# Kernel optimization log

Measured on AMD Instinct MI355X. Metric: run time of the kernel, lower is better.

The kernel has to match this reference:

```python
import jax, jax.numpy as jnp
import numpy as np

SR = 44100
D = SR * 30          # duration_samples = 1_323_000
N = 1024             # number of note events
L = 32768            # max note length in samples
W = 1024             # hann window length (module's window_length)
H = 8                # harmonics in the synth
K = 128              # FIR taps in the effect chain
LAT = 2              # time_latent_size


def setup_inputs() -> dict:
    key = jax.random.key(0)
    ks = jax.random.split(key, 10)
    freq_rad = jax.random.uniform(ks[0], (N,), jnp.float32, 0.01, 0.3)
    velocity = jax.random.uniform(ks[1], (N,), jnp.float32, 1.0, 127.0)
    starts = jax.random.randint(ks[2], (N,), 0, D - L, dtype=jnp.int32)
    lengths = jax.random.randint(ks[3], (N,), 2048, L + 1, dtype=jnp.int32)
    # time_embedder: Linear(1,32) -> ReLU -> Linear(32,LAT)
    w1 = jax.random.normal(ks[4], (1, 32), jnp.float32)
    b1 = jnp.zeros((32,), jnp.float32)
    w2 = jax.random.normal(ks[5], (32, LAT), jnp.float32) / jnp.sqrt(32.0)
    b2 = jnp.zeros((LAT,), jnp.float32)
    # synth amplitude MLP: [freq, vel, latent] (2+LAT) -> 64 -> H
    ws1 = jax.random.normal(ks[6], (2 + LAT, 64), jnp.float32)
    bs1 = jnp.zeros((64,), jnp.float32)
    ws2 = jax.random.normal(ks[7], (64, H), jnp.float32) / 8.0
    bs2 = jnp.zeros((H,), jnp.float32)
    # effect chain: causal FIR (OIW layout) + tanh
    fir = jax.random.normal(ks[8], (1, 1, K), jnp.float32) / K
    return dict(freq_rad=freq_rad, velocity=velocity,
                w1=w1, b1=b1, w2=w2, b2=b2,
                ws1=ws1, bs1=bs1, ws2=ws2, bs2=bs2, fir=fir,
                starts=starts, lengths=lengths, duration_samples=D)


def reference(freq_rad, velocity, w1, b1, w2, b2, ws1, bs1, ws2, bs2, fir,
              starts, lengths, duration_samples):
    Dn = int(duration_samples)
    t = jnp.arange(L, dtype=jnp.float32)            # [L]
    ti = jnp.arange(L, dtype=jnp.int32)             # [L]
    ends = starts + lengths
    # output_length = min(end, duration) - start, clipped to [0, L]
    out_len = jnp.clip(jnp.minimum(ends, Dn) - starts, 0, L)  # [N]
    # time latent: MLP on normalized start time
    nt = (starts.astype(jnp.float32) / Dn)[:, None]           # [N,1]
    lat = jax.nn.relu(nt @ w1 + b1) @ w2 + b2                  # [N,LAT]
    vel = (velocity / 127.0)[:, None]                          # [N,1]
    # harmonic amplitudes from tiny MLP (the 'synth')
    feat = jnp.concatenate([freq_rad[:, None], vel, lat], axis=-1)  # [N,2+LAT]
    amps = jax.nn.softplus(jax.nn.relu(feat @ ws1 + bs1) @ ws2 + bs2)  # [N,H]
    # additive synthesis; fixed small loop over harmonics, vectorized over [N,L]
    phase = freq_rad[:, None] * t[None, :]                     # [N,L]
    seg = jnp.zeros((N, L), jnp.float32)
    for hh in range(1, H + 1):
        seg = seg + amps[:, hh - 1:hh] * jnp.sin(hh * phase)
    seg = seg * vel
    # hann window (torch periodic) on the LAST W samples of each variable-length segment
    n = jnp.arange(W, dtype=jnp.float32)
    hann = 0.5 * (1.0 - jnp.cos(2.0 * jnp.pi * n / W))         # [W]
    wpos = ti[None, :] - (out_len[:, None] - W)                # [N,L]
    in_win = (wpos >= 0) & (wpos < W)
    factor = jnp.where(in_win, hann[jnp.clip(wpos, 0, W - 1)], 1.0)
    mask = (ti[None, :] < out_len[:, None]).astype(jnp.float32)  # zero past segment end
    seg = seg * factor * mask
    # effect chain: causal 128-tap FIR then tanh (masked so padding stays silent)
    y = jax.lax.conv_general_dilated(seg[:, None, :], fir,
                                     window_strides=(1,), padding=[(K - 1, 0)])
    seg = jnp.tanh(y[:, 0, :]) * mask                          # [N,L]
    # overlap-add: scatter each note into the output buffer
    idx = starts[:, None] + ti[None, :]                        # [N,L]
    valid = (ti[None, :] < out_len[:, None]) & (idx < Dn)
    contrib = jnp.where(valid, seg, 0.0)
    out = jnp.zeros((Dn,), jnp.float32).at[jnp.clip(idx, 0, Dn - 1).reshape(-1)].add(
        contrib.reshape(-1))
    return out
```

## Files before the change

### kernel.cpp

```cpp
#include <hip/hip_runtime.h>
#include <math.h>

#define LMAX  32768
#define WWIN  1024
#define KFIR  128
#define WOUT  512
#define TO    1024
#define SEGX  640
#define CPAD  656
#define NMAX  1024

typedef _Float16 v8h __attribute__((ext_vector_type(8)));
typedef _Float16 v4h __attribute__((ext_vector_type(4)));
typedef float    v4f __attribute__((ext_vector_type(4)));

__global__ __launch_bounds__(256) void params_k(
    const float* __restrict__ freq, const float* __restrict__ velo,
    const float* __restrict__ w1,  const float* __restrict__ b1,
    const float* __restrict__ w2,  const float* __restrict__ b2,
    const float* __restrict__ ws1, const float* __restrict__ bs1,
    const float* __restrict__ ws2, const float* __restrict__ bs2,
    const int* __restrict__ starts, const int* __restrict__ lengths,
    int Dn, int N,
    float* __restrict__ amps_out, int* __restrict__ outlen_out)
{
    __shared__ float s_w1[32], s_b1[32], s_w2[64], s_b2[2];
    __shared__ float s_ws1[256], s_bs1[64], s_ws2[512], s_bs2[8];

    const int tid = threadIdx.x;
    if (tid < 32)  { s_w1[tid] = w1[tid]; s_b1[tid] = b1[tid]; }
    if (tid < 64)  { s_w2[tid] = w2[tid]; s_bs1[tid] = bs1[tid]; }
    if (tid < 2)   s_b2[tid] = b2[tid];
    if (tid < 8)   s_bs2[tid] = bs2[tid];
    s_ws1[tid] = ws1[tid];
    s_ws2[tid] = ws2[tid];
    s_ws2[tid + 256] = ws2[tid + 256];
    __syncthreads();

    const int n = blockIdx.x * blockDim.x + tid;
    if (n >= N) return;

    int st  = starts[n];
    int len = lengths[n];
    int ol  = min(st + len, Dn) - st;
    ol = max(0, min(ol, LMAX));
    outlen_out[n] = ol;

    float v = velo[n] * (1.0f / 127.0f);
    float nt = (float)st / (float)Dn;

    float lat0 = s_b2[0], lat1 = s_b2[1];
    #pragma unroll
    for (int j = 0; j < 32; ++j) {
        float h = fmaxf(fmaf(nt, s_w1[j], s_b1[j]), 0.0f);
        lat0 = fmaf(h, s_w2[j * 2 + 0], lat0);
        lat1 = fmaf(h, s_w2[j * 2 + 1], lat1);
    }

    const float f0 = freq[n], f1 = v, f2 = lat0, f3 = lat1;

    float acc[8];
    #pragma unroll
    for (int h = 0; h < 8; ++h) acc[h] = s_bs2[h];
    #pragma unroll
    for (int j = 0; j < 64; ++j) {
        float a = s_bs1[j];
        a = fmaf(f0, s_ws1[0 * 64 + j], a);
        a = fmaf(f1, s_ws1[1 * 64 + j], a);
        a = fmaf(f2, s_ws1[2 * 64 + j], a);
        a = fmaf(f3, s_ws1[3 * 64 + j], a);
        a = fmaxf(a, 0.0f);
        #pragma unroll
        for (int h = 0; h < 8; ++h)
            acc[h] = fmaf(a, s_ws2[j * 8 + h], acc[h]);
    }
    #pragma unroll
    for (int h = 0; h < 8; ++h) {
        float a = acc[h];
        float sp = fmaxf(a, 0.0f) + log1pf(expf(-fabsf(a)));
        amps_out[n * 8 + h] = sp * v;
    }
}

__device__ __forceinline__ float fast_tanh(float x) {
    float e = __builtin_amdgcn_exp2f(x * 2.8853900817779268f);
    return fmaf(-2.0f, __builtin_amdgcn_rcpf(e + 1.0f), 1.0f);
}

__global__ __launch_bounds__(128, 3) void synth_gather_k(
    const float* __restrict__ freq_g, const int* __restrict__ starts,
    const float* __restrict__ amps_g, const int* __restrict__ outlen_g,
    const float* __restrict__ fir,
    float* __restrict__ out, int Dn, int N)
{
    __shared__ __align__(16) _Float16 segc[2][4][CPAD];
    __shared__ float fir_s[KFIR];
    __shared__ unsigned short note_list[NMAX];
    __shared__ int note_cnt;

    const int tid  = threadIdx.x;
    const int wid  = tid >> 6;
    const int lane = tid & 63;
    const int m    = lane & 15;
    const int quad = lane >> 4;
    const int o0   = blockIdx.x * TO;
    const int o_end = min(o0 + TO, Dn);
    const int ow   = o0 + wid * WOUT;

    fir_s[tid] = fir[tid];
    if (tid == 0) note_cnt = 0;
    __syncthreads();
    for (int j = tid; j < N; j += 128) {
        int st = starts[j];
        int ol = outlen_g[j];
        if (st < o_end && st + ol > o0) {
            int p = atomicAdd(&note_cnt, 1);
            note_list[p] = (unsigned short)j;
        }
    }
    __syncthreads();
    const int K = note_cnt;

    v8h afrag[12];
    #pragma unroll
    for (int t = 0; t < 12; ++t) {
        v8h af;
        #pragma unroll
        for (int j = 0; j < 8; ++j) {
            int idx = 32 * t + 8 * quad + j - 16 * m;
            float fv = (idx >= 0 && idx < KFIR) ? fir_s[idx] : 0.0f;
            af[j] = (_Float16)fv;
        }
        afrag[t] = af;
    }

    for (int z = lane; z < 4 * 20; z += 64) {
        int S = z / 20, off = z % 20;
        segc[wid][S][636 + off] = (_Float16)0.0f;
    }

    const _Float16* __restrict__ bbase = &segc[wid][m & 3][(m & ~3) + 8 * quad];

    float accA0 = 0.f, accA1 = 0.f, accA2 = 0.f, accA3 = 0.f;
    float accB0 = 0.f, accB1 = 0.f, accB2 = 0.f, accB3 = 0.f;

    const double inv2pi = 0.15915494309189535;
    const float4* __restrict__ amps4 = (const float4*)amps_g;

    int stN = 0, olN = 0; float fN = 0.f;
    float4 amN0 = {}, amN1 = {};
    if (K > 0) {
        const int nid = __builtin_amdgcn_readfirstlane((int)note_list[0]);
        stN = starts[nid]; olN = outlen_g[nid];
        fN = freq_g[nid];
        amN0 = amps4[nid * 2]; amN1 = amps4[nid * 2 + 1];
    }

    for (int kk = 0; kk < K; ++kk) {
        const int st = stN, ol = olN;
        const float f = fN;
        const float4 am0 = amN0, am1 = amN1;
        if (kk + 1 < K) {
            const int nid = __builtin_amdgcn_readfirstlane((int)note_list[kk + 1]);
            stN = starts[nid]; olN = outlen_g[nid];
            fN = freq_g[nid];
            amN0 = amps4[nid * 2]; amN1 = amps4[nid * 2 + 1];
        }

        const int base = ow - st;
        if (base >= ol || base + WOUT <= 0) continue;

        const float A0 = am0.x, A1 = am0.y, A2 = am0.z, A3 = am0.w;
        const float A4 = am1.x, A5 = am1.y, A6 = am1.z, A7 = am1.w;
        const double fd = (double)f;

        const int tseed = base - 127 + lane;
        double rev0 = fd * (double)tseed * inv2pi;
        float r0 = (float)(rev0 - floor(rev0));
        float s = __builtin_amdgcn_sinf(r0);
        float c = __builtin_amdgcn_cosf(r0);
        double d64 = fd * 64.0 * inv2pi;
        float r64 = (float)(d64 - floor(d64));
        const float sd = __builtin_amdgcn_sinf(r64);
        const float cd = __builtin_amdgcn_cosf(r64);
        const int wbase = ol - WWIN;

        const bool interior = (base >= 127) && (base + 513 <= wbase);

        if (interior) {
            #pragma unroll
            for (int i = 0; i < 10; ++i) {
                float tc = c + c;
                float sA = s;
                float sum = A0 * sA;
                float sB = tc * sA;              sum = fmaf(A1, sB, sum);
                float sC = fmaf(tc, sB, -sA);    sum = fmaf(A2, sC, sum);
                float sD = fmaf(tc, sC, -sB);    sum = fmaf(A3, sD, sum);
                float sE = fmaf(tc, sD, -sC);    sum = fmaf(A4, sE, sum);
                float sF = fmaf(tc, sE, -sD);    sum = fmaf(A5, sF, sum);
                float sG = fmaf(tc, sF, -sE);    sum = fmaf(A6, sG, sum);
                float sH = fmaf(tc, sG, -sF);    sum = fmaf(A7, sH, sum);
                _Float16 h = (_Float16)sum;
                const int x = lane + 64 * i;
                if (i == 0) {
                    #pragma unroll
                    for (int S = 0; S < 4; ++S)
                        if (x >= S) segc[wid][S][x - S] = h;
                } else {
                    #pragma unroll
                    for (int S = 0; S < 4; ++S)
                        segc[wid][S][x - S] = h;
                }
                float ns = fmaf(s, cd, c * sd);
                float nc = fmaf(c, cd, -(s * sd));
                s = ns; c = nc;
            }
        } else {
            #pragma unroll
            for (int i = 0; i < 10; ++i) {
                int t = tseed + 64 * i;
                float val = 0.0f;
                if (t >= 0 && t < ol) {
                    float tc = c + c;
                    float sA = s;
                    float sum = A0 * sA;
                    float sB = tc * sA;              sum = fmaf(A1, sB, sum);
                    float sC = fmaf(tc, sB, -sA);    sum = fmaf(A2, sC, sum);
                    float sD = fmaf(tc, sC, -sB);    sum = fmaf(A3, sD, sum);
                    float sE = fmaf(tc, sD, -sC);    sum = fmaf(A4, sE, sum);
                    float sF = fmaf(tc, sE, -sD);    sum = fmaf(A5, sF, sum);
                    float sG = fmaf(tc, sF, -sE);    sum = fmaf(A6, sG, sum);
                    float sH = fmaf(tc, sG, -sF);    sum = fmaf(A7, sH, sum);
                    int wpos = t - wbase;
                    float factor = 1.0f;
                    if (wpos >= 0)
                        factor = 0.5f - 0.5f * __builtin_amdgcn_cosf((float)wpos * (1.0f / WWIN));
                    val = sum * factor;
                }
                _Float16 h = (_Float16)val;
                const int x = lane + 64 * i;
                if (i == 0) {
                    #pragma unroll
                    for (int S = 0; S < 4; ++S)
                        if (x >= S) segc[wid][S][x - S] = h;
                } else {
                    #pragma unroll
                    for (int S = 0; S < 4; ++S)
                        segc[wid][S][x - S] = h;
                }
                float ns = fmaf(s, cd, c * sd);
                float nc = fmaf(c, cd, -(s * sd));
                s = ns; c = nc;
            }
        }

        v4f CA0 = {0.f, 0.f, 0.f, 0.f};
        v4f CA1 = {0.f, 0.f, 0.f, 0.f};
        v4f CB0 = {0.f, 0.f, 0.f, 0.f};
        v4f CB1 = {0.f, 0.f, 0.f, 0.f};
        #pragma unroll
        for (int t = 0; t < 6; ++t) {
            v4h lo = *(const v4h*)(bbase + 32 * t);
            v4h hi = *(const v4h*)(bbase + 32 * t + 4);
            v8h bf = __builtin_shufflevector(lo, hi, 0, 1, 2, 3, 4, 5, 6, 7);
            CA0 = __builtin_amdgcn_mfma_f32_16x16x32_f16(afrag[t], bf, CA0, 0, 0, 0);
            v4h lo2 = *(const v4h*)(bbase + 256 + 32 * t);
            v4h hi2 = *(const v4h*)(bbase + 256 + 32 * t + 4);
            v8h bf2 = __builtin_shufflevector(lo2, hi2, 0, 1, 2, 3, 4, 5, 6, 7);
            CB0 = __builtin_amdgcn_mfma_f32_16x16x32_f16(afrag[t], bf2, CB0, 0, 0, 0);
        }
        #pragma unroll
        for (int t = 6; t < 12; ++t) {
            v4h lo = *(const v4h*)(bbase + 32 * t);
            v4h hi = *(const v4h*)(bbase + 32 * t + 4);
            v8h bf = __builtin_shufflevector(lo, hi, 0, 1, 2, 3, 4, 5, 6, 7);
            CA1 = __builtin_amdgcn_mfma_f32_16x16x32_f16(afrag[t], bf, CA1, 0, 0, 0);
            v4h lo2 = *(const v4h*)(bbase + 256 + 32 * t);
            v4h hi2 = *(const v4h*)(bbase + 256 + 32 * t + 4);
            v8h bf2 = __builtin_shufflevector(lo2, hi2, 0, 1, 2, 3, 4, 5, 6, 7);
            CB1 = __builtin_amdgcn_mfma_f32_16x16x32_f16(afrag[t], bf2, CB1, 0, 0, 0);
        }

        {
            const int tb = base + 64 * quad + m;
            float y;
            y = CA0[0] + CA1[0]; if (tb +   0 >= 0 && tb +   0 < ol) accA0 += fast_tanh(y);
            y = CA0[1] + CA1[1]; if (tb +  16 >= 0 && tb +  16 < ol) accA1 += fast_tanh(y);
            y = CA0[2] + CA1[2]; if (tb +  32 >= 0 && tb +  32 < ol) accA2 += fast_tanh(y);
            y = CA0[3] + CA1[3]; if (tb +  48 >= 0 && tb +  48 < ol) accA3 += fast_tanh(y);
            y = CB0[0] + CB1[0]; if (tb + 256 >= 0 && tb + 256 < ol) accB0 += fast_tanh(y);
            y = CB0[1] + CB1[1]; if (tb + 272 >= 0 && tb + 272 < ol) accB1 += fast_tanh(y);
            y = CB0[2] + CB1[2]; if (tb + 288 >= 0 && tb + 288 < ol) accB2 += fast_tanh(y);
            y = CB0[3] + CB1[3]; if (tb + 304 >= 0 && tb + 304 < ol) accB3 += fast_tanh(y);
        }
    }

    const int ob = ow + 64 * quad + m;
    if (ob +   0 < Dn) out[ob +   0] = accA0;
    if (ob +  16 < Dn) out[ob +  16] = accA1;
    if (ob +  32 < Dn) out[ob +  32] = accA2;
    if (ob +  48 < Dn) out[ob +  48] = accA3;
    if (ob + 256 < Dn) out[ob + 256] = accB0;
    if (ob + 272 < Dn) out[ob + 272] = accB1;
    if (ob + 288 < Dn) out[ob + 288] = accB2;
    if (ob + 304 < Dn) out[ob + 304] = accB3;
}

extern "C" void kernel_launch(void* const* d_in, const int* in_sizes, int n_in,
                              void* d_out, int out_size, void* d_ws, size_t ws_size,
                              hipStream_t stream) {
    const float* freq    = (const float*)d_in[0];
    const float* velo    = (const float*)d_in[1];
    const float* w1      = (const float*)d_in[2];
    const float* b1      = (const float*)d_in[3];
    const float* w2      = (const float*)d_in[4];
    const float* b2      = (const float*)d_in[5];
    const float* ws1     = (const float*)d_in[6];
    const float* bs1     = (const float*)d_in[7];
    const float* ws2     = (const float*)d_in[8];
    const float* bs2     = (const float*)d_in[9];
    const float* fir     = (const float*)d_in[10];
    const int*   starts  = (const int*)d_in[11];
    const int*   lengths = (const int*)d_in[12];

    const int N  = in_sizes[0];
    const int Dn = out_size;
    float* out = (float*)d_out;

    float* amps   = (float*)d_ws;
    int*   outlen = (int*)((char*)d_ws + (size_t)N * 8 * sizeof(float));

    params_k<<<(N + 255) / 256, 256, 0, stream>>>(
        freq, velo, w1, b1, w2, b2, ws1, bs1, ws2, bs2,
        starts, lengths, Dn, N, amps, outlen);

    int n_tiles = (Dn + TO - 1) / TO;
    synth_gather_k<<<n_tiles, 128, 0, stream>>>(
        freq, starts, amps, outlen, fir, out, Dn, N);
}
```

Baseline: 144.0 us.

## Split notes across four waves per 512-sample tile and reduce partial sums in LDS

Before, each block had two waves, and each wave owned its own 512-sample output window and walked every overlapping note. Now a 256-thread block covers a single 512-sample tile, and its four waves take interleaved subsets of the note list. Each wave writes its partial sums to shared memory, and a final reduction after a barrier sums them before the store. The aim is to avoid two waves redundantly scanning and seeding notes that straddle both windows, and to balance the note work better. The cost is twice as many blocks, a repeated note-list scan per block, more LDS use, and an extra barrier plus reduction.

```diff
diff --git a/kernel.cpp b/kernel.cpp
--- a/kernel.cpp
+++ b/kernel.cpp
@@ -4,8 +4,7 @@
 #define LMAX  32768
 #define WWIN  1024
 #define KFIR  128
-#define WOUT  512
-#define TO    1024
+#define TO    512
 #define SEGX  640
 #define CPAD  656
 #define NMAX  1024
@@ -87,13 +86,14 @@
     return fmaf(-2.0f, __builtin_amdgcn_rcpf(e + 1.0f), 1.0f);
 }
 
-__global__ __launch_bounds__(128, 3) void synth_gather_k(
+__global__ __launch_bounds__(256, 4) void synth_gather_k(
     const float* __restrict__ freq_g, const int* __restrict__ starts,
     const float* __restrict__ amps_g, const int* __restrict__ outlen_g,
     const float* __restrict__ fir,
     float* __restrict__ out, int Dn, int N)
 {
-    __shared__ __align__(16) _Float16 segc[2][4][CPAD];
+    __shared__ __align__(16) _Float16 segc[4][4][CPAD];
+    __shared__ float red[4][TO];
     __shared__ float fir_s[KFIR];
     __shared__ unsigned short note_list[NMAX];
     __shared__ int note_cnt;
@@ -105,12 +105,11 @@
     const int quad = lane >> 4;
     const int o0   = blockIdx.x * TO;
     const int o_end = min(o0 + TO, Dn);
-    const int ow   = o0 + wid * WOUT;
-
-    fir_s[tid] = fir[tid];
+
+    if (tid < KFIR) fir_s[tid] = fir[tid];
     if (tid == 0) note_cnt = 0;
     __syncthreads();
-    for (int j = tid; j < N; j += 128) {
+    for (int j = tid; j < N; j += 256) {
         int st = starts[j];
         int ol = outlen_g[j];
         if (st < o_end && st + ol > o0) {
@@ -149,26 +148,26 @@
 
     int stN = 0, olN = 0; float fN = 0.f;
     float4 amN0 = {}, amN1 = {};
-    if (K > 0) {
-        const int nid = __builtin_amdgcn_readfirstlane((int)note_list[0]);
+    if (wid < K) {
+        const int nid = __builtin_amdgcn_readfirstlane((int)note_list[wid]);
         stN = starts[nid]; olN = outlen_g[nid];
         fN = freq_g[nid];
         amN0 = amps4[nid * 2]; amN1 = amps4[nid * 2 + 1];
     }
 
-    for (int kk = 0; kk < K; ++kk) {
+    for (int kk = wid; kk < K; kk += 4) {
         const int st = stN, ol = olN;
         const float f = fN;
         const float4 am0 = amN0, am1 = amN1;
-        if (kk + 1 < K) {
-            const int nid = __builtin_amdgcn_readfirstlane((int)note_list[kk + 1]);
+        if (kk + 4 < K) {
+            const int nid = __builtin_amdgcn_readfirstlane((int)note_list[kk + 4]);
             stN = starts[nid]; olN = outlen_g[nid];
             fN = freq_g[nid];
             amN0 = amps4[nid * 2]; amN1 = amps4[nid * 2 + 1];
         }
 
-        const int base = ow - st;
-        if (base >= ol || base + WOUT <= 0) continue;
+        const int base = o0 - st;
+        if (base >= ol || base + TO <= 0) continue;
 
         const float A0 = am0.x, A1 = am0.y, A2 = am0.z, A3 = am0.w;
         const float A4 = am1.x, A5 = am1.y, A6 = am1.z, A7 = am1.w;
@@ -295,15 +294,26 @@
         }
     }
 
-    const int ob = ow + 64 * quad + m;
-    if (ob +   0 < Dn) out[ob +   0] = accA0;
-    if (ob +  16 < Dn) out[ob +  16] = accA1;
-    if (ob +  32 < Dn) out[ob +  32] = accA2;
-    if (ob +  48 < Dn) out[ob +  48] = accA3;
-    if (ob + 256 < Dn) out[ob + 256] = accB0;
-    if (ob + 272 < Dn) out[ob + 272] = accB1;
-    if (ob + 288 < Dn) out[ob + 288] = accB2;
-    if (ob + 304 < Dn) out[ob + 304] = accB3;
+    {
+        const int p = 64 * quad + m;
+        red[wid][p +   0] = accA0;
+        red[wid][p +  16] = accA1;
+        red[wid][p +  32] = accA2;
+        red[wid][p +  48] = accA3;
+        red[wid][p + 256] = accB0;
+        red[wid][p + 272] = accB1;
+        red[wid][p + 288] = accB2;
+        red[wid][p + 304] = accB3;
+    }
+    __syncthreads();
+    {
+        int idx = tid;
+        float sum0 = red[0][idx] + red[1][idx] + red[2][idx] + red[3][idx];
+        int idx2 = tid + 256;
+        float sum1 = red[0][idx2] + red[1][idx2] + red[2][idx2] + red[3][idx2];
+        if (o0 + idx  < Dn) out[o0 + idx]  = sum0;
+        if (o0 + idx2 < Dn) out[o0 + idx2] = sum1;
+    }
 }
 
 extern "C" void kernel_launch(void* const* d_in, const int* in_sizes, int n_in,
@@ -335,6 +345,6 @@
         starts, lengths, Dn, N, amps, outlen);
 
     int n_tiles = (Dn + TO - 1) / TO;
-    synth_gather_k<<<n_tiles, 128, 0, stream>>>(
+    synth_gather_k<<<n_tiles, 256, 0, stream>>>(
         freq, starts, amps, outlen, fir, out, Dn, N);
 }
```

After: 147.3 us. +2.2%, slower.

## Fuse per-note parameter MLP into synth gather kernel with LDS-staged note batches

Applied to the files above, without the earlier changes.

Removes the separate params kernel. Each tile block now recomputes the note amplitude MLP and output length for its overlapping notes in chunks of up to 96 and stages them in shared memory. This saves one kernel launch, the dependency between the two kernels, and the per-note global loads of amplitudes inside the main loop. In exchange, the MLP is recomputed redundantly across the many tiles that share a note, and extra block barriers and shared memory are added, which may reduce occupancy.

```diff
diff --git a/kernel.cpp b/kernel.cpp
--- a/kernel.cpp
+++ b/kernel.cpp
@@ -6,97 +6,38 @@
 #define KFIR  128
 #define WOUT  512
 #define TO    1024
-#define SEGX  640
 #define CPAD  656
 #define NMAX  1024
+#define PMAX  96
 
 typedef _Float16 v8h __attribute__((ext_vector_type(8)));
 typedef _Float16 v4h __attribute__((ext_vector_type(4)));
 typedef float    v4f __attribute__((ext_vector_type(4)));
 
-__global__ __launch_bounds__(256) void params_k(
-    const float* __restrict__ freq, const float* __restrict__ velo,
+__device__ __forceinline__ float fast_tanh(float x) {
+    float e = __builtin_amdgcn_exp2f(x * 2.8853900817779268f);
+    return fmaf(-2.0f, __builtin_amdgcn_rcpf(e + 1.0f), 1.0f);
+}
+
+__global__ __launch_bounds__(128, 3) void synth_fused_k(
+    const float* __restrict__ freq_g, const float* __restrict__ velo_g,
     const float* __restrict__ w1,  const float* __restrict__ b1,
     const float* __restrict__ w2,  const float* __restrict__ b2,
     const float* __restrict__ ws1, const float* __restrict__ bs1,
     const float* __restrict__ ws2, const float* __restrict__ bs2,
+    const float* __restrict__ fir,
     const int* __restrict__ starts, const int* __restrict__ lengths,
-    int Dn, int N,
-    float* __restrict__ amps_out, int* __restrict__ outlen_out)
-{
-    __shared__ float s_w1[32], s_b1[32], s_w2[64], s_b2[2];
-    __shared__ float s_ws1[256], s_bs1[64], s_ws2[512], s_bs2[8];
-
-    const int tid = threadIdx.x;
-    if (tid < 32)  { s_w1[tid] = w1[tid]; s_b1[tid] = b1[tid]; }
-    if (tid < 64)  { s_w2[tid] = w2[tid]; s_bs1[tid] = bs1[tid]; }
-    if (tid < 2)   s_b2[tid] = b2[tid];
-    if (tid < 8)   s_bs2[tid] = bs2[tid];
-    s_ws1[tid] = ws1[tid];
-    s_ws2[tid] = ws2[tid];
-    s_ws2[tid + 256] = ws2[tid + 256];
-    __syncthreads();
-
-    const int n = blockIdx.x * blockDim.x + tid;
-    if (n >= N) return;
-
-    int st  = starts[n];
-    int len = lengths[n];
-    int ol  = min(st + len, Dn) - st;
-    ol = max(0, min(ol, LMAX));
-    outlen_out[n] = ol;
-
-    float v = velo[n] * (1.0f / 127.0f);
-    float nt = (float)st / (float)Dn;
-
-    float lat0 = s_b2[0], lat1 = s_b2[1];
-    #pragma unroll
-    for (int j = 0; j < 32; ++j) {
-        float h = fmaxf(fmaf(nt, s_w1[j], s_b1[j]), 0.0f);
-        lat0 = fmaf(h, s_w2[j * 2 + 0], lat0);
-        lat1 = fmaf(h, s_w2[j * 2 + 1], lat1);
-    }
-
-    const float f0 = freq[n], f1 = v, f2 = lat0, f3 = lat1;
-
-    float acc[8];
-    #pragma unroll
-    for (int h = 0; h < 8; ++h) acc[h] = s_bs2[h];
-    #pragma unroll
-    for (int j = 0; j < 64; ++j) {
-        float a = s_bs1[j];
-        a = fmaf(f0, s_ws1[0 * 64 + j], a);
-        a = fmaf(f1, s_ws1[1 * 64 + j], a);
-        a = fmaf(f2, s_ws1[2 * 64 + j], a);
-        a = fmaf(f3, s_ws1[3 * 64 + j], a);
-        a = fmaxf(a, 0.0f);
-        #pragma unroll
-        for (int h = 0; h < 8; ++h)
-            acc[h] = fmaf(a, s_ws2[j * 8 + h], acc[h]);
-    }
-    #pragma unroll
-    for (int h = 0; h < 8; ++h) {
-        float a = acc[h];
-        float sp = fmaxf(a, 0.0f) + log1pf(expf(-fabsf(a)));
-        amps_out[n * 8 + h] = sp * v;
-    }
-}
-
-__device__ __forceinline__ float fast_tanh(float x) {
-    float e = __builtin_amdgcn_exp2f(x * 2.8853900817779268f);
-    return fmaf(-2.0f, __builtin_amdgcn_rcpf(e + 1.0f), 1.0f);
-}
-
-__global__ __launch_bounds__(128, 3) void synth_gather_k(
-    const float* __restrict__ freq_g, const int* __restrict__ starts,
-    const float* __restrict__ amps_g, const int* __restrict__ outlen_g,
-    const float* __restrict__ fir,
     float* __restrict__ out, int Dn, int N)
 {
     __shared__ __align__(16) _Float16 segc[2][4][CPAD];
     __shared__ float fir_s[KFIR];
     __shared__ unsigned short note_list[NMAX];
     __shared__ int note_cnt;
+    __shared__ float s_w1[32], s_b1[32], s_w2[64], s_b2[2];
+    __shared__ float s_ws1[256], s_bs1[64], s_ws2[512], s_bs2[8];
+    __shared__ int   stl[PMAX], oll[PMAX];
+    __shared__ float fl[PMAX];
+    __shared__ __align__(16) float ampsl[PMAX][8];
 
     const int tid  = threadIdx.x;
     const int wid  = tid >> 6;
@@ -108,11 +49,21 @@
     const int ow   = o0 + wid * WOUT;
 
     fir_s[tid] = fir[tid];
+    if (tid < 32) { s_w1[tid] = w1[tid]; s_b1[tid] = b1[tid]; }
+    if (tid < 64) { s_w2[tid] = w2[tid]; s_bs1[tid] = bs1[tid]; }
+    if (tid < 2)  s_b2[tid] = b2[tid];
+    if (tid < 8)  s_bs2[tid] = bs2[tid];
+    s_ws1[tid] = ws1[tid];       s_ws1[tid + 128] = ws1[tid + 128];
+    s_ws2[tid] = ws2[tid];       s_ws2[tid + 128] = ws2[tid + 128];
+    s_ws2[tid + 256] = ws2[tid + 256]; s_ws2[tid + 384] = ws2[tid + 384];
     if (tid == 0) note_cnt = 0;
     __syncthreads();
+
     for (int j = tid; j < N; j += 128) {
         int st = starts[j];
-        int ol = outlen_g[j];
+        int len = lengths[j];
+        int ol = min(st + len, Dn) - st;
+        ol = max(0, min(ol, LMAX));
         if (st < o_end && st + ol > o0) {
             int p = atomicAdd(&note_cnt, 1);
             note_list[p] = (unsigned short)j;
@@ -145,83 +96,84 @@
     float accB0 = 0.f, accB1 = 0.f, accB2 = 0.f, accB3 = 0.f;
 
     const double inv2pi = 0.15915494309189535;
-    const float4* __restrict__ amps4 = (const float4*)amps_g;
-
-    int stN = 0, olN = 0; float fN = 0.f;
-    float4 amN0 = {}, amN1 = {};
-    if (K > 0) {
-        const int nid = __builtin_amdgcn_readfirstlane((int)note_list[0]);
-        stN = starts[nid]; olN = outlen_g[nid];
-        fN = freq_g[nid];
-        amN0 = amps4[nid * 2]; amN1 = amps4[nid * 2 + 1];
-    }
-
-    for (int kk = 0; kk < K; ++kk) {
-        const int st = stN, ol = olN;
-        const float f = fN;
-        const float4 am0 = amN0, am1 = amN1;
-        if (kk + 1 < K) {
-            const int nid = __builtin_amdgcn_readfirstlane((int)note_list[kk + 1]);
-            stN = starts[nid]; olN = outlen_g[nid];
-            fN = freq_g[nid];
-            amN0 = amps4[nid * 2]; amN1 = amps4[nid * 2 + 1];
+
+    for (int c = 0; c < K; c += PMAX) {
+        const int kn = min(K - c, PMAX);
+
+        __syncthreads();
+        if (tid < kn) {
+            const int nid = (int)note_list[c + tid];
+            int st  = starts[nid];
+            int len = lengths[nid];
+            int ol  = min(st + len, Dn) - st;
+            ol = max(0, min(ol, LMAX));
+            stl[tid] = st;
+            oll[tid] = ol;
+            float v = velo_g[nid] * (1.0f / 127.0f);
+            float f = freq_g[nid];
+            fl[tid] = f;
+            float nt = (float)st / (float)Dn;
+            float lat0 = s_b2[0], lat1 = s_b2[1];
+            #pragma unroll
+            for (int j = 0; j < 32; ++j) {
+                float h = fmaxf(fmaf(nt, s_w1[j], s_b1[j]), 0.0f);
+                lat0 = fmaf(h, s_w2[j * 2 + 0], lat0);
+                lat1 = fmaf(h, s_w2[j * 2 + 1], lat1);
+            }
+            float acc[8];
+            #pragma unroll
+            for (int h = 0; h < 8; ++h) acc[h] = s_bs2[h];
+            #pragma unroll
+            for (int j = 0; j < 64; ++j) {
+                float a = s_bs1[j];
+                a = fmaf(f,    s_ws1[0 * 64 + j], a);
+                a = fmaf(v,    s_ws1[1 * 64 + j], a);
+                a = fmaf(lat0, s_ws1[2 * 64 + j], a);
+                a = fmaf(lat1, s_ws1[3 * 64 + j], a);
+                a = fmaxf(a, 0.0f);
+                #pragma unroll
+                for (int h = 0; h < 8; ++h)
+                    acc[h] = fmaf(a, s_ws2[j * 8 + h], acc[h]);
+            }
+            #pragma unroll
+            for (int h = 0; h < 8; ++h) {
+                float a = acc[h];
+                float sp = fmaxf(a, 0.0f) + log1pf(expf(-fabsf(a)));
+                ampsl[tid][h] = sp * v;
+            }
         }
-
-        const int base = ow - st;
-        if (base >= ol || base + WOUT <= 0) continue;
-
-        const float A0 = am0.x, A1 = am0.y, A2 = am0.z, A3 = am0.w;
-        const float A4 = am1.x, A5 = am1.y, A6 = am1.z, A7 = am1.w;
-        const double fd = (double)f;
-
-        const int tseed = base - 127 + lane;
-        double rev0 = fd * (double)tseed * inv2pi;
-        float r0 = (float)(rev0 - floor(rev0));
-        float s = __builtin_amdgcn_sinf(r0);
-        float c = __builtin_amdgcn_cosf(r0);
-        double d64 = fd * 64.0 * inv2pi;
-        float r64 = (float)(d64 - floor(d64));
-        const float sd = __builtin_amdgcn_sinf(r64);
-        const float cd = __builtin_amdgcn_cosf(r64);
-        const int wbase = ol - WWIN;
-
-        const bool interior = (base >= 127) && (base + 513 <= wbase);
-
-        if (interior) {
-            #pragma unroll
-            for (int i = 0; i < 10; ++i) {
-                float tc = c + c;
-                float sA = s;
-                float sum = A0 * sA;
-                float sB = tc * sA;              sum = fmaf(A1, sB, sum);
-                float sC = fmaf(tc, sB, -sA);    sum = fmaf(A2, sC, sum);
-                float sD = fmaf(tc, sC, -sB);    sum = fmaf(A3, sD, sum);
-                float sE = fmaf(tc, sD, -sC);    sum = fmaf(A4, sE, sum);
-                float sF = fmaf(tc, sE, -sD);    sum = fmaf(A5, sF, sum);
-                float sG = fmaf(tc, sF, -sE);    sum = fmaf(A6, sG, sum);
-                float sH = fmaf(tc, sG, -sF);    sum = fmaf(A7, sH, sum);
-                _Float16 h = (_Float16)sum;
-                const int x = lane + 64 * i;
-                if (i == 0) {
-                    #pragma unroll
-                    for (int S = 0; S < 4; ++S)
-                        if (x >= S) segc[wid][S][x - S] = h;
-                } else {
-                    #pragma unroll
-                    for (int S = 0; S < 4; ++S)
-                        segc[wid][S][x - S] = h;
-                }
-                float ns = fmaf(s, cd, c * sd);
-                float nc = fmaf(c, cd, -(s * sd));
-                s = ns; c = nc;
-            }
-        } else {
-            #pragma unroll
-            for (int i = 0; i < 10; ++i) {
-                int t = tseed + 64 * i;
-                float val = 0.0f;
-                if (t >= 0 && t < ol) {
-                    float tc = c + c;
+        __syncthreads();
+
+        for (int kk = 0; kk < kn; ++kk) {
+            const int st = stl[kk];
+            const int ol = oll[kk];
+            const int base = ow - st;
+            if (base >= ol || base + WOUT <= 0) continue;
+
+            const float f = fl[kk];
+            const float4 am0 = *(const float4*)&ampsl[kk][0];
+            const float4 am1 = *(const float4*)&ampsl[kk][4];
+            const float A0 = am0.x, A1 = am0.y, A2 = am0.z, A3 = am0.w;
+            const float A4 = am1.x, A5 = am1.y, A6 = am1.z, A7 = am1.w;
+            const double fd = (double)f;
+
+            const int tseed = base - 127 + lane;
+            double rev0 = fd * (double)tseed * inv2pi;
+            float r0 = (float)(rev0 - floor(rev0));
+            float s = __builtin_amdgcn_sinf(r0);
+            float cc = __builtin_amdgcn_cosf(r0);
+            double d64 = fd * 64.0 * inv2pi;
+            float r64 = (float)(d64 - floor(d64));
+            const float sd = __builtin_amdgcn_sinf(r64);
+            const float cd = __builtin_amdgcn_cosf(r64);
+            const int wbase = ol - WWIN;
+
+            const bool interior = (base >= 127) && (base + 513 <= wbase);
+
+            if (interior) {
+                #pragma unroll
+                for (int i = 0; i < 10; ++i) {
+                    float tc = cc + cc;
                     float sA = s;
                     float sum = A0 * sA;
                     float sB = tc * sA;              sum = fmaf(A1, sB, sum);
@@ -231,67 +183,99 @@
                     float sF = fmaf(tc, sE, -sD);    sum = fmaf(A5, sF, sum);
                     float sG = fmaf(tc, sF, -sE);    sum = fmaf(A6, sG, sum);
                     float sH = fmaf(tc, sG, -sF);    sum = fmaf(A7, sH, sum);
-                    int wpos = t - wbase;
-                    float factor = 1.0f;
-                    if (wpos >= 0)
-                        factor = 0.5f - 0.5f * __builtin_amdgcn_cosf((float)wpos * (1.0f / WWIN));
-                    val = sum * factor;
+                    _Float16 h = (_Float16)sum;
+                    const int x = lane + 64 * i;
+                    if (i == 0) {
+                        #pragma unroll
+                        for (int S = 0; S < 4; ++S)
+                            if (x >= S) segc[wid][S][x - S] = h;
+                    } else {
+                        #pragma unroll
+                        for (int S = 0; S < 4; ++S)
+                            segc[wid][S][x - S] = h;
+                    }
+                    float ns = fmaf(s, cd, cc * sd);
+                    float nc = fmaf(cc, cd, -(s * sd));
+                    s = ns; cc = nc;
                 }
-                _Float16 h = (_Float16)val;
-                const int x = lane + 64 * i;
-                if (i == 0) {
-                    #pragma unroll
-                    for (int S = 0; S < 4; ++S)
-                        if (x >= S) segc[wid][S][x - S] = h;
-                } else {
-                    #pragma unroll
-                    for (int S = 0; S < 4; ++S)
-                        segc[wid][S][x - S] = h;
+            } else {
+                #pragma unroll
+                for (int i = 0; i < 10; ++i) {
+                    int t = tseed + 64 * i;
+                    float val = 0.0f;
+                    if (t >= 0 && t < ol) {
+                        float tc = cc + cc;
+                        float sA = s;
+                        float sum = A0 * sA;
+                        float sB = tc * sA;              sum = fmaf(A1, sB, sum);
+                        float sC = fmaf(tc, sB, -sA);    sum = fmaf(A2, sC, sum);
+                        float sD = fmaf(tc, sC, -sB);    sum = fmaf(A3, sD, sum);
+                        float sE = fmaf(tc, sD, -sC);    sum = fmaf(A4, sE, sum);
+                        float sF = fmaf(tc, sE, -sD);    sum = fmaf(A5, sF, sum);
+                        float sG = fmaf(tc, sF, -sE);    sum = fmaf(A6, sG, sum);
+                        float sH = fmaf(tc, sG, -sF);    sum = fmaf(A7, sH, sum);
+                        int wpos = t - wbase;
+                        float factor = 1.0f;
+                        if (wpos >= 0)
+                            factor = 0.5f - 0.5f * __builtin_amdgcn_cosf((float)wpos * (1.0f / WWIN));
+                        val = sum * factor;
+                    }
+                    _Float16 h = (_Float16)val;
+                    const int x = lane + 64 * i;
+                    if (i == 0) {
+                        #pragma unroll
+                        for (int S = 0; S < 4; ++S)
+                            if (x >= S) segc[wid][S][x - S] = h;
+                    } else {
+                        #pragma unroll
+                        for (int S = 0; S < 4; ++S)
+                            segc[wid][S][x - S] = h;
+                    }
+                    float ns = fmaf(s, cd, cc * sd);
+                    float nc = fmaf(cc, cd, -(s * sd));
+                    s = ns; cc = nc;
                 }
-                float ns = fmaf(s, cd, c * sd);
-                float nc = fmaf(c, cd, -(s * sd));
-                s = ns; c = nc;
-            }
-        }
-
-        v4f CA0 = {0.f, 0.f, 0.f, 0.f};
-        v4f CA1 = {0.f, 0.f, 0.f, 0.f};
-        v4f CB0 = {0.f, 0.f, 0.f, 0.f};
-        v4f CB1 = {0.f, 0.f, 0.f, 0.f};
-        #pragma unroll
-        for (int t = 0; t < 6; ++t) {
-            v4h lo = *(const v4h*)(bbase + 32 * t);
-            v4h hi = *(const v4h*)(bbase + 32 * t + 4);
-            v8h bf = __builtin_shufflevector(lo, hi, 0, 1, 2, 3, 4, 5, 6, 7);
-            CA0 = __builtin_amdgcn_mfma_f32_16x16x32_f16(afrag[t], bf, CA0, 0, 0, 0);
-            v4h lo2 = *(const v4h*)(bbase + 256 + 32 * t);
-            v4h hi2 = *(const v4h*)(bbase + 256 + 32 * t + 4);
-            v8h bf2 = __builtin_shufflevector(lo2, hi2, 0, 1, 2, 3, 4, 5, 6, 7);
-            CB0 = __builtin_amdgcn_mfma_f32_16x16x32_f16(afrag[t], bf2, CB0, 0, 0, 0);
-        }
-        #pragma unroll
-        for (int t = 6; t < 12; ++t) {
-            v4h lo = *(const v4h*)(bbase + 32 * t);
-            v4h hi = *(const v4h*)(bbase + 32 * t + 4);
-            v8h bf = __builtin_shufflevector(lo, hi, 0, 1, 2, 3, 4, 5, 6, 7);
-            CA1 = __builtin_amdgcn_mfma_f32_16x16x32_f16(afrag[t], bf, CA1, 0, 0, 0);
-            v4h lo2 = *(const v4h*)(bbase + 256 + 32 * t);
-            v4h hi2 = *(const v4h*)(bbase + 256 + 32 * t + 4);
-            v8h bf2 = __builtin_shufflevector(lo2, hi2, 0, 1, 2, 3, 4, 5, 6, 7);
-            CB1 = __builtin_amdgcn_mfma_f32_16x16x32_f16(afrag[t], bf2, CB1, 0, 0, 0);
-        }
-
-        {
-            const int tb = base + 64 * quad + m;
-            float y;
-            y = CA0[0] + CA1[0]; if (tb +   0 >= 0 && tb +   0 < ol) accA0 += fast_tanh(y);
-            y = CA0[1] + CA1[1]; if (tb +  16 >= 0 && tb +  16 < ol) accA1 += fast_tanh(y);
-            y = CA0[2] + CA1[2]; if (tb +  32 >= 0 && tb +  32 < ol) accA2 += fast_tanh(y);
-            y = CA0[3] + CA1[3]; if (tb +  48 >= 0 && tb +  48 < ol) accA3 += fast_tanh(y);
-            y = CB0[0] + CB1[0]; if (tb + 256 >= 0 && tb + 256 < ol) accB0 += fast_tanh(y);
-            y = CB0[1] + CB1[1]; if (tb + 272 >= 0 && tb + 272 < ol) accB1 += fast_tanh(y);
-            y = CB0[2] + CB1[2]; if (tb + 288 >= 0 && tb + 288 < ol) accB2 += fast_tanh(y);
-            y = CB0[3] + CB1[3]; if (tb + 304 >= 0 && tb + 304 < ol) accB3 += fast_tanh(y);
+            }
+
+            v4f CA0 = {0.f, 0.f, 0.f, 0.f};
+            v4f CA1 = {0.f, 0.f, 0.f, 0.f};
+            v4f CB0 = {0.f, 0.f, 0.f, 0.f};
+            v4f CB1 = {0.f, 0.f, 0.f, 0.f};
+            #pragma unroll
+            for (int t = 0; t < 6; ++t) {
+                v4h lo = *(const v4h*)(bbase + 32 * t);
+                v4h hi = *(const v4h*)(bbase + 32 * t + 4);
+                v8h bf = __builtin_shufflevector(lo, hi, 0, 1, 2, 3, 4, 5, 6, 7);
+                CA0 = __builtin_amdgcn_mfma_f32_16x16x32_f16(afrag[t], bf, CA0, 0, 0, 0);
+                v4h lo2 = *(const v4h*)(bbase + 256 + 32 * t);
+                v4h hi2 = *(const v4h*)(bbase + 256 + 32 * t + 4);
+                v8h bf2 = __builtin_shufflevector(lo2, hi2, 0, 1, 2, 3, 4, 5, 6, 7);
+                CB0 = __builtin_amdgcn_mfma_f32_16x16x32_f16(afrag[t], bf2, CB0, 0, 0, 0);
+            }
+            #pragma unroll
+            for (int t = 6; t < 12; ++t) {
+                v4h lo = *(const v4h*)(bbase + 32 * t);
+                v4h hi = *(const v4h*)(bbase + 32 * t + 4);
+                v8h bf = __builtin_shufflevector(lo, hi, 0, 1, 2, 3, 4, 5, 6, 7);
+                CA1 = __builtin_amdgcn_mfma_f32_16x16x32_f16(afrag[t], bf, CA1, 0, 0, 0);
+                v4h lo2 = *(const v4h*)(bbase + 256 + 32 * t);
+                v4h hi2 = *(const v4h*)(bbase + 256 + 32 * t + 4);
+                v8h bf2 = __builtin_shufflevector(lo2, hi2, 0, 1, 2, 3, 4, 5, 6, 7);
+                CB1 = __builtin_amdgcn_mfma_f32_16x16x32_f16(afrag[t], bf2, CB1, 0, 0, 0);
+            }
+
+            {
+                const int tb = base + 64 * quad + m;
+                float y;
+                y = CA0[0] + CA1[0]; if (tb +   0 >= 0 && tb +   0 < ol) accA0 += fast_tanh(y);
+                y = CA0[1] + CA1[1]; if (tb +  16 >= 0 && tb +  16 < ol) accA1 += fast_tanh(y);
+                y = CA0[2] + CA1[2]; if (tb +  32 >= 0 && tb +  32 < ol) accA2 += fast_tanh(y);
+                y = CA0[3] + CA1[3]; if (tb +  48 >= 0 && tb +  48 < ol) accA3 += fast_tanh(y);
+                y = CB0[0] + CB1[0]; if (tb + 256 >= 0 && tb + 256 < ol) accB0 += fast_tanh(y);
+                y = CB0[1] + CB1[1]; if (tb + 272 >= 0 && tb + 272 < ol) accB1 += fast_tanh(y);
+                y = CB0[2] + CB1[2]; if (tb + 288 >= 0 && tb + 288 < ol) accB2 += fast_tanh(y);
+                y = CB0[3] + CB1[3]; if (tb + 304 >= 0 && tb + 304 < ol) accB3 += fast_tanh(y);
+            }
         }
     }
 
@@ -327,14 +311,8 @@
     const int Dn = out_size;
     float* out = (float*)d_out;
 
-    float* amps   = (float*)d_ws;
-    int*   outlen = (int*)((char*)d_ws + (size_t)N * 8 * sizeof(float));
-
-    params_k<<<(N + 255) / 256, 256, 0, stream>>>(
+    int n_tiles = (Dn + TO - 1) / TO;
+    synth_fused_k<<<n_tiles, 128, 0, stream>>>(
         freq, velo, w1, b1, w2, b2, ws1, bs1, ws2, bs2,
-        starts, lengths, Dn, N, amps, outlen);
-
-    int n_tiles = (Dn + TO - 1) / TO;
-    synth_gather_k<<<n_tiles, 128, 0, stream>>>(
-        freq, starts, amps, outlen, fir, out, Dn, N);
+        fir, starts, lengths, out, Dn, N);
 }
```

New measurement: 144.9 us. Within noise of the previous version (+0.6%).
